# Kernel optimization log

Measured on AMD Instinct MI355X. Metric: run time of the kernel, lower is better.

## Reference

```python
import jax, jax.numpy as jnp
import numpy as np

L, D, H, FF = 4, 256, 8, 4 * 256  # num_layers, d_model, nhead, ffn hidden
DK = D // H
EPS = 1e-5


def _ln(x, g, b):
    mu = jnp.mean(x, axis=-1, keepdims=True)
    var = jnp.mean(jnp.square(x - mu), axis=-1, keepdims=True)
    return (x - mu) * jax.lax.rsqrt(var + EPS) * g + b


def setup_inputs() -> dict:
    key = jax.random.key(0)
    ks = jax.random.split(key, 16)
    B, N = 8, 1024
    s = 0.02
    return {
        "x": jax.random.normal(ks[0], (B, N, D), jnp.float32),
        "coords": jax.random.normal(ks[1], (B, N, 3), jnp.float32),
        "Wq": jax.random.normal(ks[2], (L, D, D), jnp.float32) * s,
        "bq": jnp.zeros((L, D), jnp.float32),
        "Wk": jax.random.normal(ks[3], (L, D, D), jnp.float32) * s,
        "bk": jnp.zeros((L, D), jnp.float32),
        "Wv": jax.random.normal(ks[4], (L, D, D), jnp.float32) * s,
        "bv": jnp.zeros((L, D), jnp.float32),
        "alpha": jnp.full((L,), 0.1, jnp.float32),
        "W1": jax.random.normal(ks[5], (L, D, FF), jnp.float32) * s,
        "b1": jnp.zeros((L, FF), jnp.float32),
        "W2": jax.random.normal(ks[6], (L, FF, D), jnp.float32) * s,
        "b2": jnp.zeros((L, D), jnp.float32),
        "g1": jnp.ones((L, D), jnp.float32),
        "be1": jnp.zeros((L, D), jnp.float32),
        "g2": jnp.ones((L, D), jnp.float32),
        "be2": jnp.zeros((L, D), jnp.float32),
    }


def reference(x, coords, Wq, bq, Wk, bk, Wv, bv, alpha, W1, b1, W2, b2, g1, be1, g2, be2):
    B, N, _ = x.shape
    # Per-batch pairwise coord dot products (same math as the BN x BN matmul
    # sliced per batch in the original, computed without the cross-batch waste).
    G0 = jnp.einsum("bnc,bmc->bnm", coords, coords)  # [B,N,N]
    scale = 1.0 / jnp.sqrt(jnp.float32(DK))
    for i in range(L):
        q = (x @ Wq[i] + bq[i]).reshape(B, N, H, DK)
        k = (x @ Wk[i] + bk[i]).reshape(B, N, H, DK)
        v = (x @ Wv[i] + bv[i]).reshape(B, N, H, DK)
        scores = jnp.einsum("bnhd,bmhd->bhnm", q, k) * scale + (alpha[i] * G0)[:, None]
        attn = jax.nn.softmax(scores, axis=-1)
        out = jnp.einsum("bhnm,bmhd->bnhd", attn, v).reshape(B, N, D)
        x = _ln(x + out, g1[i], be1[i])
        ff = jnp.maximum(x @ W1[i] + b1[i], 0.0) @ W2[i] + b2[i]
        x = _ln(x + ff, g2[i], be2[i])
    return x
```

## Files before the change

kernel.cpp:

```cpp
#include <hip/hip_runtime.h>
#include <hip/hip_bf16.h>

#define BB 8
#define NN 1024
#define DD 256
#define HH 8
#define DK 32
#define FFN 1024
#define NLAYERS 4
#define MM (BB * NN)
#define ROW_ELEMS (MM * DD)

#define QSCALE 0.2550655192922103f
#define LOG2E  1.4426950408889634f

typedef unsigned short ushort_t;
typedef __attribute__((ext_vector_type(8))) short bf16x8;
typedef __attribute__((ext_vector_type(4))) short bf16x4;
typedef __attribute__((ext_vector_type(4))) float f32x4;

__device__ __forceinline__ f32x4 mfma16(bf16x4 a, bf16x4 b, f32x4 c) {
#if __has_builtin(__builtin_amdgcn_mfma_f32_16x16x16bf16_1k)
    return __builtin_amdgcn_mfma_f32_16x16x16bf16_1k(a, b, c, 0, 0, 0);
#elif defined(__AMDGCN__)
    f32x4 d;
    asm volatile("v_mfma_f32_16x16x16_bf16 %0, %1, %2, %3"
                 : "=v"(d)
                 : "v"(a), "v"(b), "v"(c));
    return d;
#else
    return c;
#endif
}

__device__ __forceinline__ ushort_t f2b(float f) {
    __hip_bfloat16 h = __float2bfloat16(f);
    return *reinterpret_cast<ushort_t*>(&h);
}

__device__ __forceinline__ float fast_exp2(float x) {
#if __has_builtin(__builtin_amdgcn_exp2f)
    return __builtin_amdgcn_exp2f(x);
#else
    return exp2f(x);
#endif
}

__device__ __forceinline__ void async_ld16(const void* g, void* l) {
    __builtin_amdgcn_global_load_lds((const __attribute__((address_space(1))) void*)g,
                                     (__attribute__((address_space(3))) void*)l, 16, 0, 0);
}

__global__ __launch_bounds__(256) void copy_in_kernel(const float4* __restrict__ in,
                                                      float4* __restrict__ xf,
                                                      ushort4* __restrict__ xb, int n4,
                                                      const float* __restrict__ coords,
                                                      ushort_t* __restrict__ Qa,
                                                      ushort_t* __restrict__ Ka) {
    int i = blockIdx.x * 256 + threadIdx.x;
    if (i < n4) {
        float4 v = in[i];
        xf[i] = v;
        ushort4 b = {f2b(v.x), f2b(v.y), f2b(v.z), f2b(v.w)};
        xb[i] = b;
    }
    if (blockIdx.x < 256) {
        const int id = blockIdx.x * 256 + threadIdx.x;
        const int bh = id >> 10, n = id & 1023;
        const int b = bh >> 3;
        ushort_t buf[32];
#pragma unroll
        for (int d = 0; d < 32; ++d) buf[d] = 0;
        buf[0] = f2b(coords[(size_t)(b * NN + n) * 3 + 0]);
        buf[1] = f2b(coords[(size_t)(b * NN + n) * 3 + 1]);
        buf[2] = f2b(coords[(size_t)(b * NN + n) * 3 + 2]);
        ushort_t* kp = Ka + ((size_t)bh * NN + n) * 64 + 32;
        ushort_t* qp = Qa + ((size_t)bh * NN + n) * 64 + 32;
        const uint4* b4 = (const uint4*)buf;
        uint4 z4 = {0u, 0u, 0u, 0u};
#pragma unroll
        for (int c = 0; c < 4; ++c) {
            *(uint4*)(kp + c * 8) = b4[c];
            *(uint4*)(qp + c * 8) = z4;
        }
    }
}

__global__ __launch_bounds__(256) void prep_kernel(const float* __restrict__ Wq,
                                                   const float* __restrict__ Wk,
                                                   const float* __restrict__ Wv,
                                                   const float* __restrict__ W1,
                                                   const float* __restrict__ W2,
                                                   const float* __restrict__ bq,
                                                   const float* __restrict__ bk,
                                                   const float* __restrict__ bv,
                                                   ushort_t* __restrict__ wqkvt,
                                                   ushort_t* __restrict__ w1t,
                                                   ushort_t* __restrict__ w2t,
                                                   float* __restrict__ bqkv) {
    const int id = blockIdx.x;
    const int layer = id / 707;
    const int r = id % 707;
    const int tid = threadIdx.x;

    if (r >= 704) {
        const int chunk = r - 704;
        const float* src = (chunk == 0) ? bq : (chunk == 1) ? bk : bv;
        bqkv[layer * 768 + chunk * 256 + tid] = src[layer * 256 + tid];
        return;
    }

    const float* src;
    ushort_t* dst;
    int R, C, x, y;
    if (r < 192) {
        const int w = r >> 6, rr = r & 63;
        src = ((w == 0) ? Wq : (w == 1) ? Wk : Wv) + (size_t)layer * 65536;
        dst = wqkvt + (size_t)layer * 196608 + w * 65536;
        R = 256; C = 256; x = rr & 7; y = rr >> 3;
    } else if (r < 448) {
        const int rr = r - 192;
        src = W1 + (size_t)layer * 262144;
        dst = w1t + (size_t)layer * 262144;
        R = 256; C = 1024; x = rr & 31; y = rr >> 5;
    } else {
        const int rr = r - 448;
        src = W2 + (size_t)layer * 262144;
        dst = w2t + (size_t)layer * 262144;
        R = 1024; C = 256; x = rr & 7; y = rr >> 3;
    }
    const int r0 = y * 32, c0 = x * 32;
    __shared__ float tile[32][33];
    const int tx = tid & 31, ty = tid >> 5;
#pragma unroll
    for (int i = 0; i < 4; ++i)
        tile[ty + 8 * i][tx] = src[(size_t)(r0 + ty + 8 * i) * C + (c0 + tx)];
    __syncthreads();
#pragma unroll
    for (int i = 0; i < 4; ++i)
        dst[(size_t)(c0 + ty + 8 * i) * R + (r0 + tx)] = f2b(tile[tx][ty + 8 * i]);
}

template <int MODE, int BM>
__global__ __launch_bounds__(256) void mfma_gemm_kernel(const ushort_t* __restrict__ A,
                                                        const ushort_t* __restrict__ Bt,
                                                        const float* __restrict__ bias,
                                                        void* __restrict__ C0,
                                                        void* __restrict__ C1,
                                                        void* __restrict__ C2,
                                                        const float* __restrict__ coords,
                                                        const float* __restrict__ alpha, int layer,
                                                        int K, int ldc) {
    constexpr int NI = BM / 32;
    __shared__ ushort_t As0[2][BM * 32];
    __shared__ ushort_t As1[2][BM * 32];
    __shared__ ushort_t Bs0[2][128 * 32];
    __shared__ ushort_t Bs1[2][128 * 32];

    const int t    = threadIdx.x;
    const int bm   = blockIdx.y * BM;
    const int bn   = blockIdx.x * 128;
    const int wave = t >> 6, lane = t & 63;
    const int wm   = (wave >> 1) * (BM / 2), wn = (wave & 1) * 64;
    const int quad = lane >> 4, l16 = lane & 15;

    const int srow = t >> 2;
    const int scol = (t & 3) * 8;

    f32x4 acc[NI][4];
#pragma unroll
    for (int i = 0; i < NI; ++i)
#pragma unroll
        for (int j = 0; j < 4; ++j) {
            f32x4 z = {0.f, 0.f, 0.f, 0.f};
            acc[i][j] = z;
        }

    auto stage = [&](int pb, int k0) {
        async_ld16(A + (size_t)(bm + srow) * K + k0 + scol, As0[pb] + wave * 512);
        if constexpr (BM == 128)
            async_ld16(A + (size_t)(bm + 64 + srow) * K + k0 + scol, As0[pb] + 2048 + wave * 512);
        async_ld16(Bt + (size_t)(bn + srow) * K + k0 + scol, Bs0[pb] + wave * 512);
        async_ld16(Bt + (size_t)(bn + 64 + srow) * K + k0 + scol, Bs0[pb] + 2048 + wave * 512);
        async_ld16(A + (size_t)(bm + srow) * K + k0 + 32 + scol, As1[pb] + wave * 512);
        if constexpr (BM == 128)
            async_ld16(A + (size_t)(bm + 64 + srow) * K + k0 + 32 + scol, As1[pb] + 2048 + wave * 512);
        async_ld16(Bt + (size_t)(bn + srow) * K + k0 + 32 + scol, Bs1[pb] + wave * 512);
        async_ld16(Bt + (size_t)(bn + 64 + srow) * K + k0 + 32 + scol, Bs1[pb] + 2048 + wave * 512);
    };

    stage(0, 0);
    int pb = 0;
    for (int k0 = 0; k0 < K; k0 += 64, pb ^= 1) {
        __syncthreads();

        if (k0 + 64 < K) stage(pb ^ 1, k0 + 64);

        bf16x8 af0[NI], af1[NI], bf0[4], bf1[4];
#pragma unroll
        for (int i = 0; i < NI; ++i) {
            af0[i] = *(const bf16x8*)(As0[pb] + (wm + i * 16 + l16) * 32 + quad * 8);
            af1[i] = *(const bf16x8*)(As1[pb] + (wm + i * 16 + l16) * 32 + quad * 8);
        }
#pragma unroll
        for (int j = 0; j < 4; ++j) {
            bf0[j] = *(const bf16x8*)(Bs0[pb] + (wn + j * 16 + l16) * 32 + quad * 8);
            bf1[j] = *(const bf16x8*)(Bs1[pb] + (wn + j * 16 + l16) * 32 + quad * 8);
        }
#pragma unroll
        for (int i = 0; i < NI; ++i)
#pragma unroll
            for (int j = 0; j < 4; ++j) {
                acc[i][j] = __builtin_amdgcn_mfma_f32_16x16x32_bf16(af0[i], bf0[j], acc[i][j], 0, 0, 0);
                acc[i][j] = __builtin_amdgcn_mfma_f32_16x16x32_bf16(af1[i], bf1[j], acc[i][j], 0, 0, 0);
            }
    }

    const float av = (MODE == 2) ? alpha[layer] : 0.f;

#pragma unroll
    for (int j = 0; j < 4; ++j) {
        const int col = bn + wn + j * 16 + l16;
        const float bsv = bias[col];
#pragma unroll
        for (int i = 0; i < NI; ++i) {
            const int row0 = bm + wm + i * 16 + quad * 4;
            if (MODE == 2) {
                const int bb2 = row0 >> 10, nn0 = row0 & 1023;
                const int which = col >> 8, rem = col & 255;
                const int h = rem >> 5, d = rem & 31;
                const size_t bh = (size_t)((bb2 << 3) + h);
                if (which == 2) {
                    ushort4 pk;
                    pk.x = f2b(acc[i][j][0] + bsv);
                    pk.y = f2b(acc[i][j][1] + bsv);
                    pk.z = f2b(acc[i][j][2] + bsv);
                    pk.w = f2b(acc[i][j][3] + bsv);
                    *(ushort4*)&((ushort_t*)C2)[(bh * DK + d) * NN + nn0] = pk;
                } else {
#pragma unroll
                    for (int r = 0; r < 4; ++r) {
                        const float v = acc[i][j][r] + bsv;
                        const int nn = nn0 + r;
                        if (which == 0) {
                            ((ushort_t*)C0)[(bh * NN + nn) * 64 + d] = f2b(v * QSCALE);
                            if (d < 3)
                                ((ushort_t*)C0)[(bh * NN + nn) * 64 + 32 + d] =
                                    f2b(av * LOG2E * coords[(size_t)(bb2 * NN + nn) * 3 + d]);
                        } else {
                            ((ushort_t*)C1)[(bh * NN + nn) * 64 + d] = f2b(v);
                        }
                    }
                }
            } else {
#pragma unroll
                for (int r = 0; r < 4; ++r) {
                    float v = acc[i][j][r] + bsv;
                    if (MODE == 0)
                        ((float*)C0)[(size_t)(row0 + r) * ldc + col] = v;
                    else
                        ((ushort_t*)C0)[(size_t)(row0 + r) * ldc + col] = f2b(fmaxf(v, 0.f));
                }
            }
        }
    }
}

template <int DO_QKV>
__global__ __launch_bounds__(512) void ffn_ln_kernel(const float* __restrict__ aout,
                                                     const float* __restrict__ xfin,
                                                     const ushort_t* __restrict__ W1t,
                                                     const ushort_t* __restrict__ W2t,
                                                     const float* __restrict__ g1,
                                                     const float* __restrict__ be1,
                                                     const float* __restrict__ b1,
                                                     const float* __restrict__ b2,
                                                     const float* __restrict__ g2,
                                                     const float* __restrict__ be2,
                                                     float* __restrict__ xout,
                                                     const ushort_t* __restrict__ Wqkvt,
                                                     const float* __restrict__ bqkv,
                                                     const float* __restrict__ coords,
                                                     const float* __restrict__ alpha, int qlayer,
                                                     ushort_t* __restrict__ Qa,
                                                     ushort_t* __restrict__ Ka,
                                                     ushort_t* __restrict__ Vt) {
    __shared__ ushort_t Ha[8][32][32];
    __shared__ ushort_t Asf[8][32][32];
    __shared__ ushort_t Bs0[2][256 * 32];
    __shared__ ushort_t Bs1[2][256 * 32];
    __shared__ float Ya[32][260];
    __shared__ float redS[8][32];
    __shared__ float redQ[8][32];

    const int t = threadIdx.x;
    const int bm = blockIdx.x * 32;
    const int wave = t >> 6, lane = t & 63;
    const int quad = lane >> 4, l16 = lane & 15;
    const int wn = wave * 32;
    const int scol = (t & 3) * 8;

    auto stageB1 = [&](int pb, int nc, int ks) {
        const int nbase = nc * 256;
        const int k0 = ks * 64;
#pragma unroll
        for (int c = 0; c < 2; ++c) {
            const int brow = nbase + c * 128 + (t >> 2);
            async_ld16(W1t + (size_t)brow * 256 + k0 + scol, Bs0[pb] + c * 4096 + wave * 512);
            async_ld16(W1t + (size_t)brow * 256 + k0 + 32 + scol, Bs1[pb] + c * 4096 + wave * 512);
        }
    };
    auto stageB2 = [&](int pb, int nc, int ks) {
        const int k0 = nc * 256 + ks * 64;
#pragma unroll
        for (int c = 0; c < 2; ++c) {
            const int brow = c * 128 + (t >> 2);
            async_ld16(W2t + (size_t)brow * 1024 + k0 + scol, Bs0[pb] + c * 4096 + wave * 512);
            async_ld16(W2t + (size_t)brow * 1024 + k0 + 32 + scol, Bs1[pb] + c * 4096 + wave * 512);
        }
    };
    auto stage = [&](int pb, int st) {
        const int group = st >> 2, ks = st & 3, nc = group >> 1;
        if (!(group & 1)) stageB1(pb, nc, ks);
        else stageB2(pb, nc, ks);
    };
    auto stageQKV = [&](int pb, int qst) {
        const int chunk = qst >> 2, ks = qst & 3;
#pragma unroll
        for (int c = 0; c < 2; ++c) {
            const int brow = chunk * 256 + c * 128 + (t >> 2);
            async_ld16(Wqkvt + (size_t)brow * 256 + ks * 64 + scol, Bs0[pb] + c * 4096 + wave * 512);
            async_ld16(Wqkvt + (size_t)brow * 256 + ks * 64 + 32 + scol, Bs1[pb] + c * 4096 + wave * 512);
        }
    };

    stage(0, 0);

#pragma unroll
    for (int rr = 0; rr < 4; ++rr) {
        const int row = wave * 4 + rr;
        const size_t base = (size_t)(bm + row) * DD + lane * 4;

        float4 xv = *(const float4*)(xfin + base);
        float4 dl = *(const float4*)(aout + base);
        float v0 = xv.x + dl.x, v1 = xv.y + dl.y, v2 = xv.z + dl.z, v3 = xv.w + dl.w;

        float s = v0 + v1 + v2 + v3;
#pragma unroll
        for (int off = 32; off; off >>= 1) s += __shfl_xor(s, off);
        const float mean = s * (1.0f / 256.0f);

        float d0 = v0 - mean, d1 = v1 - mean, d2 = v2 - mean, d3 = v3 - mean;
        float s2 = d0 * d0 + d1 * d1 + d2 * d2 + d3 * d3;
#pragma unroll
        for (int off = 32; off; off >>= 1) s2 += __shfl_xor(s2, off);
        const float rs = rsqrtf(s2 * (1.0f / 256.0f) + 1e-5f);

        float4 gv = *(const float4*)(g1 + lane * 4);
        float4 bv = *(const float4*)(be1 + lane * 4);
        float y0 = d0 * rs * gv.x + bv.x;
        float y1 = d1 * rs * gv.y + bv.y;
        float y2 = d2 * rs * gv.z + bv.z;
        float y3 = d3 * rs * gv.w + bv.w;

        float4 yv = {y0, y1, y2, y3};
        *(float4*)&Ya[row][lane * 4] = yv;
        const int col0 = lane * 4;
        ushort4 yb = {f2b(y0), f2b(y1), f2b(y2), f2b(y3)};
        *(ushort4*)&Asf[col0 >> 5][row][col0 & 31] = yb;
    }

    f32x4 acc1[2][2], acc2[2][2];
#pragma unroll
    for (int i = 0; i < 2; ++i)
#pragma unroll
        for (int j = 0; j < 2; ++j) {
            f32x4 z = {0.f, 0.f, 0.f, 0.f};
            acc1[i][j] = z;
            acc2[i][j] = z;
        }

    int pb = 0;
    for (int st = 0; st < 32; ++st, pb ^= 1) {
        __syncthreads();
        if (st < 31) stage(pb ^ 1, st + 1);
        else if (DO_QKV) stageQKV(pb ^ 1, 0);

        const int group = st >> 2, ks = st & 3;
        const bool ff1 = !(group & 1);

        bf16x8 af0[2], af1[2], bf0[2], bf1[2];
#pragma unroll
        for (int i = 0; i < 2; ++i) {
            if (ff1) {
                af0[i] = *(const bf16x8*)&Asf[2 * ks][i * 16 + l16][quad * 8];
                af1[i] = *(const bf16x8*)&Asf[2 * ks + 1][i * 16 + l16][quad * 8];
            } else {
                af0[i] = *(const bf16x8*)&Ha[2 * ks][i * 16 + l16][quad * 8];
                af1[i] = *(const bf16x8*)&Ha[2 * ks + 1][i * 16 + l16][quad * 8];
            }
        }
#pragma unroll
        for (int j = 0; j < 2; ++j) {
            bf0[j] = *(const bf16x8*)(Bs0[pb] + (wn + j * 16 + l16) * 32 + quad * 8);
            bf1[j] = *(const bf16x8*)(Bs1[pb] + (wn + j * 16 + l16) * 32 + quad * 8);
        }

        if (ff1) {
#pragma unroll
            for (int i = 0; i < 2; ++i)
#pragma unroll
                for (int j = 0; j < 2; ++j) {
                    acc1[i][j] = __builtin_amdgcn_mfma_f32_16x16x32_bf16(af0[i], bf0[j], acc1[i][j], 0, 0, 0);
                    acc1[i][j] = __builtin_amdgcn_mfma_f32_16x16x32_bf16(af1[i], bf1[j], acc1[i][j], 0, 0, 0);
                }
            if (ks == 3) {
                const int nc = group >> 1;
#pragma unroll
                for (int j = 0; j < 2; ++j) {
                    const int col = nc * 256 + wn + j * 16 + l16;
                    const float bj = b1[col];
#pragma unroll
                    for (int i = 0; i < 2; ++i)
#pragma unroll
                        for (int r = 0; r < 4; ++r) {
                            const int row = i * 16 + quad * 4 + r;
                            Ha[wave][row][j * 16 + l16] =
                                f2b(fmaxf(acc1[i][j][r] + bj, 0.f));
                        }
                }
#pragma unroll
                for (int i = 0; i < 2; ++i)
#pragma unroll
                    for (int j = 0; j < 2; ++j) {
                        f32x4 z = {0.f, 0.f, 0.f, 0.f};
                        acc1[i][j] = z;
                    }
            }
        } else {
#pragma unroll
            for (int i = 0; i < 2; ++i)
#pragma unroll
                for (int j = 0; j < 2; ++j) {
                    acc2[i][j] = __builtin_amdgcn_mfma_f32_16x16x32_bf16(af0[i], bf0[j], acc2[i][j], 0, 0, 0);
                    acc2[i][j] = __builtin_amdgcn_mfma_f32_16x16x32_bf16(af1[i], bf1[j], acc2[i][j], 0, 0, 0);
                }
        }
    }

    float mean[2][4], rstd[2][4];

    {
        float sum_[2][4];
#pragma unroll
        for (int i = 0; i < 2; ++i)
#pragma unroll
            for (int r = 0; r < 4; ++r) sum_[i][r] = 0.f;
#pragma unroll
        for (int j = 0; j < 2; ++j) {
            const int col = wn + j * 16 + l16;
            const float bj = b2[col];
#pragma unroll
            for (int i = 0; i < 2; ++i) {
#pragma unroll
                for (int r = 0; r < 4; ++r) {
                    const int row = i * 16 + quad * 4 + r;
                    const float v = acc2[i][j][r] + bj + Ya[row][col];
                    acc2[i][j][r] = v;
                    sum_[i][r] += v;
                }
            }
        }
#pragma unroll
        for (int i = 0; i < 2; ++i)
#pragma unroll
            for (int r = 0; r < 4; ++r) {
                float s = sum_[i][r];
                s += __shfl_xor(s, 1);
                s += __shfl_xor(s, 2);
                s += __shfl_xor(s, 4);
                s += __shfl_xor(s, 8);
                sum_[i][r] = s;
            }
        if (l16 == 0) {
#pragma unroll
            for (int i = 0; i < 2; ++i)
#pragma unroll
                for (int r = 0; r < 4; ++r) redS[wave][i * 16 + quad * 4 + r] = sum_[i][r];
        }
        __syncthreads();
#pragma unroll
        for (int i = 0; i < 2; ++i)
#pragma unroll
            for (int r = 0; r < 4; ++r) {
                const int rl = i * 16 + quad * 4 + r;
                float s = 0.f;
#pragma unroll
                for (int w = 0; w < 8; ++w) s += redS[w][rl];
                mean[i][r] = s * (1.0f / 256.0f);
            }
    }

    {
        float sq_[2][4];
#pragma unroll
        for (int i = 0; i < 2; ++i)
#pragma unroll
            for (int r = 0; r < 4; ++r) sq_[i][r] = 0.f;
#pragma unroll
        for (int j = 0; j < 2; ++j)
#pragma unroll
            for (int i = 0; i < 2; ++i)
#pragma unroll
                for (int r = 0; r < 4; ++r) {
                    const float d = acc2[i][j][r] - mean[i][r];
                    sq_[i][r] += d * d;
                }
#pragma unroll
        for (int i = 0; i < 2; ++i)
#pragma unroll
            for (int r = 0; r < 4; ++r) {
                float s = sq_[i][r];
                s += __shfl_xor(s, 1);
                s += __shfl_xor(s, 2);
                s += __shfl_xor(s, 4);
                s += __shfl_xor(s, 8);
                sq_[i][r] = s;
            }
        if (l16 == 0) {
#pragma unroll
            for (int i = 0; i < 2; ++i)
#pragma unroll
                for (int r = 0; r < 4; ++r) redQ[wave][i * 16 + quad * 4 + r] = sq_[i][r];
        }
        __syncthreads();
#pragma unroll
        for (int i = 0; i < 2; ++i)
#pragma unroll
            for (int r = 0; r < 4; ++r) {
                const int rl = i * 16 + quad * 4 + r;
                float s = 0.f;
#pragma unroll
                for (int w = 0; w < 8; ++w) s += redQ[w][rl];
                rstd[i][r] = rsqrtf(s * (1.0f / 256.0f) + 1e-5f);
            }
    }

#pragma unroll
    for (int j = 0; j < 2; ++j) {
        const int col = wn + j * 16 + l16;
        const float gv = g2[col];
        const float bev = be2[col];
#pragma unroll
        for (int i = 0; i < 2; ++i) {
            const int row = bm + i * 16 + quad * 4;
#pragma unroll
            for (int r = 0; r < 4; ++r) {
                const float y = (acc2[i][j][r] - mean[i][r]) * rstd[i][r] * gv + bev;
                xout[(size_t)(row + r) * DD + col] = y;
                if (DO_QKV)
                    Asf[wave][i * 16 + quad * 4 + r][j * 16 + l16] = f2b(y);
            }
        }
    }

    if constexpr (DO_QKV) {
        const float av = alpha[qlayer];
        f32x4 acc3[2][2];
#pragma unroll
        for (int i = 0; i < 2; ++i)
#pragma unroll
            for (int j = 0; j < 2; ++j) {
                f32x4 z = {0.f, 0.f, 0.f, 0.f};
                acc3[i][j] = z;
            }

        for (int qst = 0; qst < 12; ++qst, pb ^= 1) {
            __syncthreads();
            if (qst < 11) stageQKV(pb ^ 1, qst + 1);

            const int ks = qst & 3;
            bf16x8 af0[2], af1[2], bf0[2], bf1[2];
#pragma unroll
            for (int i = 0; i < 2; ++i) {
                af0[i] = *(const bf16x8*)&Asf[2 * ks][i * 16 + l16][quad * 8];
                af1[i] = *(const bf16x8*)&Asf[2 * ks + 1][i * 16 + l16][quad * 8];
            }
#pragma unroll
            for (int j = 0; j < 2; ++j) {
                bf0[j] = *(const bf16x8*)(Bs0[pb] + (wn + j * 16 + l16) * 32 + quad * 8);
                bf1[j] = *(const bf16x8*)(Bs1[pb] + (wn + j * 16 + l16) * 32 + quad * 8);
            }
#pragma unroll
            for (int i = 0; i < 2; ++i)
#pragma unroll
                for (int j = 0; j < 2; ++j) {
                    acc3[i][j] = __builtin_amdgcn_mfma_f32_16x16x32_bf16(af0[i], bf0[j], acc3[i][j], 0, 0, 0);
                    acc3[i][j] = __builtin_amdgcn_mfma_f32_16x16x32_bf16(af1[i], bf1[j], acc3[i][j], 0, 0, 0);
                }

            if (ks == 3) {
                const int which = qst >> 2;
#pragma unroll
                for (int j = 0; j < 2; ++j) {
                    const int rem = wn + j * 16 + l16;
                    const float bsv = bqkv[which * 256 + rem];
                    const int h = rem >> 5, d = rem & 31;
#pragma unroll
                    for (int i = 0; i < 2; ++i) {
                        const int row0 = bm + i * 16 + quad * 4;
                        const int bb2 = row0 >> 10, nn0 = row0 & 1023;
                        const size_t bh = (size_t)((bb2 << 3) + h);
                        if (which == 2) {
                            ushort4 pk;
                            pk.x = f2b(acc3[i][j][0] + bsv);
                            pk.y = f2b(acc3[i][j][1] + bsv);
                            pk.z = f2b(acc3[i][j][2] + bsv);
                            pk.w = f2b(acc3[i][j][3] + bsv);
                            *(ushort4*)&Vt[(bh * DK + d) * NN + nn0] = pk;
                        } else {
#pragma unroll
                            for (int r = 0; r < 4; ++r) {
                                const float v = acc3[i][j][r] + bsv;
                                const int nn = nn0 + r;
                                if (which == 0) {
                                    Qa[(bh * NN + nn) * 64 + d] = f2b(v * QSCALE);
                                    if (d < 3)
                                        Qa[(bh * NN + nn) * 64 + 32 + d] =
                                            f2b(av * LOG2E *
                                                coords[(size_t)(bb2 * NN + nn) * 3 + d]);
                                } else {
                                    Ka[(bh * NN + nn) * 64 + d] = f2b(v);
                                }
                            }
                        }
                    }
                }
#pragma unroll
                for (int i = 0; i < 2; ++i)
#pragma unroll
                    for (int j = 0; j < 2; ++j) {
                        f32x4 z = {0.f, 0.f, 0.f, 0.f};
                        acc3[i][j] = z;
                    }
            }
        }
    }
}

__global__ __launch_bounds__(256, 2) void attn8_kernel(const ushort_t* __restrict__ Qa,
                                                       const ushort_t* __restrict__ Ka,
                                                       const ushort_t* __restrict__ Vt,
                                                       float* __restrict__ aout) {
    const int b = blockIdx.x, h = blockIdx.y, n0 = blockIdx.z * 64;
    const int t = threadIdx.x, wave = t >> 6, lane = t & 63;
    const int quad = lane >> 4, l16 = lane & 15;
    const int bh = b * HH + h;

    __shared__ __align__(16) char smem[56320];
    ushort_t (*Ks)[64][72] = (ushort_t (*)[64][72])smem;
    ushort_t (*Vs)[32][72] = (ushort_t (*)[32][72])(smem + 36864);
    float    (*Om)[64][36] = (float (*)[64][36])smem;
    float    (*Lm)[64]     = (float (*)[64])(smem + 55296);

    bf16x8 aq[4][2];
#pragma unroll
    for (int s = 0; s < 4; ++s) {
        const ushort_t* qp = Qa + ((size_t)bh * NN + n0 + s * 16 + l16) * 64 + quad * 8;
        aq[s][0] = *(const bf16x8*)qp;
        aq[s][1] = *(const bf16x8*)(qp + 32);
    }

    const f32x4 z = {0.f, 0.f, 0.f, 0.f};
    f32x4 acc[4][2];
    float lsum[4];
#pragma unroll
    for (int s = 0; s < 4; ++s) { acc[s][0] = z; acc[s][1] = z; lsum[s] = 0.f; }

    const ushort_t* kg = Ka + ((size_t)bh * NN + wave * 256) * 64;
    const ushort_t* vg = Vt + (size_t)bh * DK * NN + wave * 256;

    const int srow = lane >> 3, sch = (lane & 7) * 8;

    uint4 kreg[8], vreg[4];
#pragma unroll
    for (int i = 0; i < 8; ++i) kreg[i] = *(const uint4*)(kg + (size_t)(i * 8 + srow) * 64 + sch);
#pragma unroll
    for (int i = 0; i < 4; ++i) vreg[i] = *(const uint4*)(vg + (size_t)(i * 8 + srow) * NN + sch);

    for (int kt = 0; kt < 4; ++kt) {
#pragma unroll
        for (int i = 0; i < 8; ++i) *(uint4*)&Ks[wave][i * 8 + srow][sch] = kreg[i];
#pragma unroll
        for (int i = 0; i < 4; ++i) *(uint4*)&Vs[wave][i * 8 + srow][sch] = vreg[i];

        bf16x8 bk0[4], bk1[4];
#pragma unroll
        for (int jt = 0; jt < 4; ++jt) {
            bk0[jt] = *(const bf16x8*)&Ks[wave][jt * 16 + l16][quad * 8];
            bk1[jt] = *(const bf16x8*)&Ks[wave][jt * 16 + l16][32 + quad * 8];
        }
        bf16x4 vfrag[2][4];
#pragma unroll
        for (int g = 0; g < 2; ++g)
#pragma unroll
            for (int jt = 0; jt < 4; ++jt)
                vfrag[g][jt] = *(const bf16x4*)&Vs[wave][g * 16 + l16][jt * 16 + quad * 4];

        if (kt < 3) {
            const ushort_t* kg2 = kg + (size_t)(kt + 1) * 64 * 64;
            const ushort_t* vg2 = vg + (kt + 1) * 64;
#pragma unroll
            for (int i = 0; i < 8; ++i)
                kreg[i] = *(const uint4*)(kg2 + (size_t)(i * 8 + srow) * 64 + sch);
#pragma unroll
            for (int i = 0; i < 4; ++i)
                vreg[i] = *(const uint4*)(vg2 + (size_t)(i * 8 + srow) * NN + sch);
        }

#pragma unroll
        for (int s = 0; s < 4; ++s) {
            f32x4 st[4];
            __builtin_amdgcn_s_setprio(1);
#pragma unroll
            for (int jt = 0; jt < 4; ++jt) {
                st[jt] = __builtin_amdgcn_mfma_f32_16x16x32_bf16(bk0[jt], aq[s][0], z, 0, 0, 0);
                st[jt] = __builtin_amdgcn_mfma_f32_16x16x32_bf16(bk1[jt], aq[s][1], st[jt], 0, 0, 0);
            }
            __builtin_amdgcn_s_setprio(0);
            bf16x4 pf[4];
            float ls = 0.f;
#pragma unroll
            for (int jt = 0; jt < 4; ++jt) {
                float e0 = fast_exp2(st[jt][0]);
                float e1 = fast_exp2(st[jt][1]);
                float e2 = fast_exp2(st[jt][2]);
                float e3 = fast_exp2(st[jt][3]);
                ls += (e0 + e1) + (e2 + e3);
                pf[jt][0] = (short)f2b(e0);
                pf[jt][1] = (short)f2b(e1);
                pf[jt][2] = (short)f2b(e2);
                pf[jt][3] = (short)f2b(e3);
            }
            lsum[s] += ls;
            __builtin_amdgcn_s_setprio(1);
#pragma unroll
            for (int jt = 0; jt < 4; ++jt) {
                acc[s][0] = mfma16(vfrag[0][jt], pf[jt], acc[s][0]);
                acc[s][1] = mfma16(vfrag[1][jt], pf[jt], acc[s][1]);
            }
            __builtin_amdgcn_s_setprio(0);
        }
    }

#pragma unroll
    for (int s = 0; s < 4; ++s) {
        lsum[s] += __shfl_xor(lsum[s], 16);
        lsum[s] += __shfl_xor(lsum[s], 32);
    }

    __syncthreads();
    if (quad == 0) {
#pragma unroll
        for (int s = 0; s < 4; ++s) Lm[wave][s * 16 + l16] = lsum[s];
    }

#pragma unroll
    for (int s = 0; s < 4; ++s) {
        const int q = s * 16 + l16;
#pragma unroll
        for (int g = 0; g < 2; ++g) {
            float4 v = {acc[s][g][0], acc[s][g][1], acc[s][g][2], acc[s][g][3]};
            *(float4*)&Om[wave][q][g * 16 + quad * 4] = v;
        }
    }
    __syncthreads();

    {
        const int q = t >> 2, dseg = (t & 3) * 8;
        const float inv = 1.0f / (Lm[0][q] + Lm[1][q] + Lm[2][q] + Lm[3][q]);
        float* op = aout + (size_t)(b * NN + n0 + q) * DD + h * DK + dseg;
        float4 s0 = {0.f, 0.f, 0.f, 0.f}, s1 = {0.f, 0.f, 0.f, 0.f};
#pragma unroll
        for (int w = 0; w < 4; ++w) {
            float4 a = *(const float4*)&Om[w][q][dseg];
            float4 c = *(const float4*)&Om[w][q][dseg + 4];
            s0.x += a.x; s0.y += a.y; s0.z += a.z; s0.w += a.w;
            s1.x += c.x; s1.y += c.y; s1.z += c.z; s1.w += c.w;
        }
        float4 o0 = {s0.x * inv, s0.y * inv, s0.z * inv, s0.w * inv};
        float4 o1 = {s1.x * inv, s1.y * inv, s1.z * inv, s1.w * inv};
        *(float4*)op = o0;
        *(float4*)(op + 4) = o1;
    }
}

extern "C" void kernel_launch(void* const* d_in, const int* in_sizes, int n_in,
                              void* d_out, int out_size, void* d_ws, size_t ws_size,
                              hipStream_t stream) {
    const float* x      = (const float*)d_in[0];
    const float* coords = (const float*)d_in[1];
    const float* Wq     = (const float*)d_in[2];
    const float* bq     = (const float*)d_in[3];
    const float* Wk     = (const float*)d_in[4];
    const float* bk     = (const float*)d_in[5];
    const float* Wv     = (const float*)d_in[6];
    const float* bv     = (const float*)d_in[7];
    const float* alpha  = (const float*)d_in[8];
    const float* W1     = (const float*)d_in[9];
    const float* b1     = (const float*)d_in[10];
    const float* W2     = (const float*)d_in[11];
    const float* b2     = (const float*)d_in[12];
    const float* g1     = (const float*)d_in[13];
    const float* be1    = (const float*)d_in[14];
    const float* g2     = (const float*)d_in[15];
    const float* be2    = (const float*)d_in[16];

    float* ws = (float*)d_ws;
    float*    xf    = ws;
    ushort_t* xb    = (ushort_t*)(ws + 2097152);
    ushort_t* Qa    = (ushort_t*)(ws + 3145728);
    ushort_t* Ka    = (ushort_t*)(ws + 5242880);
    ushort_t* Vt    = (ushort_t*)(ws + 7340032);
    float*    aout  = ws + 8388608;
    ushort_t* wqkvt = (ushort_t*)(ws + 10485760);
    ushort_t* w1t   = (ushort_t*)(ws + 10878976);
    ushort_t* w2t   = (ushort_t*)(ws + 11403264);
    float*    bqkv  = ws + 11927552;

    prep_kernel<<<NLAYERS * 707, 256, 0, stream>>>(Wq, Wk, Wv, W1, W2, bq, bk, bv,
                                                   wqkvt, w1t, w2t, bqkv);

    copy_in_kernel<<<ROW_ELEMS / 4 / 256, 256, 0, stream>>>(
        (const float4*)x, (float4*)xf, (ushort4*)xb, ROW_ELEMS / 4, coords, Qa, Ka);

    mfma_gemm_kernel<2, 64><<<dim3(6, 128), 256, 0, stream>>>(
        xb, wqkvt, bqkv, Qa, Ka, Vt, coords, alpha, 0, 256, 0);

    for (int i = 0; i < NLAYERS; ++i) {
        attn8_kernel<<<dim3(8, 8, 16), 256, 0, stream>>>(Qa, Ka, Vt, aout);

        if (i < NLAYERS - 1) {
            ffn_ln_kernel<1><<<MM / 32, 512, 0, stream>>>(
                aout, xf, w1t + (size_t)i * 262144, w2t + (size_t)i * 262144,
                g1 + i * 256, be1 + i * 256, b1 + i * 1024, b2 + i * 256,
                g2 + i * 256, be2 + i * 256, xf,
                wqkvt + (size_t)(i + 1) * 196608, bqkv + (i + 1) * 768,
                coords, alpha, i + 1, Qa, Ka, Vt);
        } else {
            ffn_ln_kernel<0><<<MM / 32, 512, 0, stream>>>(
                aout, xf, w1t + (size_t)i * 262144, w2t + (size_t)i * 262144,
                g1 + i * 256, be1 + i * 256, b1 + i * 1024, b2 + i * 256,
                g2 + i * 256, be2 + i * 256, (float*)d_out,
                nullptr, nullptr, nullptr, nullptr, 0, nullptr, nullptr, nullptr);
        }
    }
}
```

Before: 363.4 us.

## Triple-buffer weight staging in fused FFN/QKV kernel with partial vmcnt waits

Moves the FFN and QKV weight streaming from a double-buffered to a triple-buffered LDS pipeline, issuing loads two stages ahead. It replaces full __syncthreads with explicit s_waitcnt vmcnt(4) barriers, so the in-flight prefetch for the next stage is not drained each iteration. To fit the extra buffer in LDS, the reduction scratch is aliased onto the Ha array and the Ya padding is dropped. This risks LDS bank conflicts from the unpadded Ya rows and correctness problems if the vmcnt counting or the aliasing of Ha is wrong. The larger LDS footprint could also lower occupancy.

```diff
diff --git a/kernel.cpp b/kernel.cpp
--- a/kernel.cpp
+++ b/kernel.cpp
@@ -49,6 +49,21 @@
 __device__ __forceinline__ void async_ld16(const void* g, void* l) {
     __builtin_amdgcn_global_load_lds((const __attribute__((address_space(1))) void*)g,
                                      (__attribute__((address_space(3))) void*)l, 16, 0, 0);
+}
+
+__device__ __forceinline__ void pipe_barrier4() {
+#if defined(__AMDGCN__)
+    asm volatile("s_waitcnt vmcnt(4) lgkmcnt(0)" ::: "memory");
+#endif
+    __builtin_amdgcn_s_barrier();
+    __builtin_amdgcn_sched_barrier(0);
+}
+__device__ __forceinline__ void pipe_barrier0() {
+#if defined(__AMDGCN__)
+    asm volatile("s_waitcnt vmcnt(0) lgkmcnt(0)" ::: "memory");
+#endif
+    __builtin_amdgcn_s_barrier();
+    __builtin_amdgcn_sched_barrier(0);
 }
 
 __global__ __launch_bounds__(256) void copy_in_kernel(const float4* __restrict__ in,
@@ -287,11 +302,11 @@
                                                      ushort_t* __restrict__ Vt) {
     __shared__ ushort_t Ha[8][32][32];
     __shared__ ushort_t Asf[8][32][32];
-    __shared__ ushort_t Bs0[2][256 * 32];
-    __shared__ ushort_t Bs1[2][256 * 32];
-    __shared__ float Ya[32][260];
-    __shared__ float redS[8][32];
-    __shared__ float redQ[8][32];
+    __shared__ ushort_t Bs0[3][8192];
+    __shared__ ushort_t Bs1[3][8192];
+    __shared__ float Ya[32][256];
+    float* redS = (float*)&Ha[0][0][0];
+    float* redQ = redS + 256;
 
     const int t = threadIdx.x;
     const int bm = blockIdx.x * 32;
@@ -300,41 +315,42 @@
     const int wn = wave * 32;
     const int scol = (t & 3) * 8;
 
-    auto stageB1 = [&](int pb, int nc, int ks) {
+    auto stageB1 = [&](int buf, int nc, int ks) {
         const int nbase = nc * 256;
         const int k0 = ks * 64;
 #pragma unroll
         for (int c = 0; c < 2; ++c) {
             const int brow = nbase + c * 128 + (t >> 2);
-            async_ld16(W1t + (size_t)brow * 256 + k0 + scol, Bs0[pb] + c * 4096 + wave * 512);
-            async_ld16(W1t + (size_t)brow * 256 + k0 + 32 + scol, Bs1[pb] + c * 4096 + wave * 512);
+            async_ld16(W1t + (size_t)brow * 256 + k0 + scol, Bs0[buf] + c * 4096 + wave * 512);
+            async_ld16(W1t + (size_t)brow * 256 + k0 + 32 + scol, Bs1[buf] + c * 4096 + wave * 512);
         }
     };
-    auto stageB2 = [&](int pb, int nc, int ks) {
+    auto stageB2 = [&](int buf, int nc, int ks) {
         const int k0 = nc * 256 + ks * 64;
 #pragma unroll
         for (int c = 0; c < 2; ++c) {
             const int brow = c * 128 + (t >> 2);
-            async_ld16(W2t + (size_t)brow * 1024 + k0 + scol, Bs0[pb] + c * 4096 + wave * 512);
-            async_ld16(W2t + (size_t)brow * 1024 + k0 + 32 + scol, Bs1[pb] + c * 4096 + wave * 512);
+            async_ld16(W2t + (size_t)brow * 1024 + k0 + scol, Bs0[buf] + c * 4096 + wave * 512);
+            async_ld16(W2t + (size_t)brow * 1024 + k0 + 32 + scol, Bs1[buf] + c * 4096 + wave * 512);
         }
     };
-    auto stage = [&](int pb, int st) {
+    auto stageFFN = [&](int buf, int st) {
         const int group = st >> 2, ks = st & 3, nc = group >> 1;
-        if (!(group & 1)) stageB1(pb, nc, ks);
-        else stageB2(pb, nc, ks);
+        if (!(group & 1)) stageB1(buf, nc, ks);
+        else stageB2(buf, nc, ks);
     };
-    auto stageQKV = [&](int pb, int qst) {
+    auto stageQKV = [&](int buf, int qst) {
         const int chunk = qst >> 2, ks = qst & 3;
 #pragma unroll
         for (int c = 0; c < 2; ++c) {
             const int brow = chunk * 256 + c * 128 + (t >> 2);
-            async_ld16(Wqkvt + (size_t)brow * 256 + ks * 64 + scol, Bs0[pb] + c * 4096 + wave * 512);
-            async_ld16(Wqkvt + (size_t)brow * 256 + ks * 64 + 32 + scol, Bs1[pb] + c * 4096 + wave * 512);
+            async_ld16(Wqkvt + (size_t)brow * 256 + ks * 64 + scol, Bs0[buf] + c * 4096 + wave * 512);
+            async_ld16(Wqkvt + (size_t)brow * 256 + ks * 64 + 32 + scol, Bs1[buf] + c * 4096 + wave * 512);
         }
     };
 
-    stage(0, 0);
+    stageFFN(0, 0);
+    stageFFN(1, 1);
 
 #pragma unroll
     for (int rr = 0; rr < 4; ++rr) {
@@ -380,12 +396,15 @@
             acc2[i][j] = z;
         }
 
-    int pb = 0;
-    for (int st = 0; st < 32; ++st, pb ^= 1) {
-        __syncthreads();
-        if (st < 31) stage(pb ^ 1, st + 1);
-        else if (DO_QKV) stageQKV(pb ^ 1, 0);
-
+    for (int st = 0; st < 32; ++st) {
+        if (!DO_QKV && st == 31) pipe_barrier0();
+        else pipe_barrier4();
+
+        const int nxt = st + 2;
+        if (nxt < 32) stageFFN(nxt % 3, nxt);
+        else if (DO_QKV && nxt < 34) stageQKV(nxt % 3, nxt - 32);
+
+        const int buf = st % 3;
         const int group = st >> 2, ks = st & 3;
         const bool ff1 = !(group & 1);
 
@@ -402,8 +421,8 @@
         }
 #pragma unroll
         for (int j = 0; j < 2; ++j) {
-            bf0[j] = *(const bf16x8*)(Bs0[pb] + (wn + j * 16 + l16) * 32 + quad * 8);
-            bf1[j] = *(const bf16x8*)(Bs1[pb] + (wn + j * 16 + l16) * 32 + quad * 8);
+            bf0[j] = *(const bf16x8*)(Bs0[buf] + (wn + j * 16 + l16) * 32 + quad * 8);
+            bf1[j] = *(const bf16x8*)(Bs1[buf] + (wn + j * 16 + l16) * 32 + quad * 8);
         }
 
         if (ff1) {
@@ -449,6 +468,8 @@
     }
 
     float mean[2][4], rstd[2][4];
+
+    __syncthreads();
 
     {
         float sum_[2][4];
@@ -486,7 +507,7 @@
 #pragma unroll
             for (int i = 0; i < 2; ++i)
 #pragma unroll
-                for (int r = 0; r < 4; ++r) redS[wave][i * 16 + quad * 4 + r] = sum_[i][r];
+                for (int r = 0; r < 4; ++r) redS[wave * 32 + i * 16 + quad * 4 + r] = sum_[i][r];
         }
         __syncthreads();
 #pragma unroll
@@ -496,7 +517,7 @@
                 const int rl = i * 16 + quad * 4 + r;
                 float s = 0.f;
 #pragma unroll
-                for (int w = 0; w < 8; ++w) s += redS[w][rl];
+                for (int w = 0; w < 8; ++w) s += redS[w * 32 + rl];
                 mean[i][r] = s * (1.0f / 256.0f);
             }
     }
@@ -531,7 +552,7 @@
 #pragma unroll
             for (int i = 0; i < 2; ++i)
 #pragma unroll
-                for (int r = 0; r < 4; ++r) redQ[wave][i * 16 + quad * 4 + r] = sq_[i][r];
+                for (int r = 0; r < 4; ++r) redQ[wave * 32 + i * 16 + quad * 4 + r] = sq_[i][r];
         }
         __syncthreads();
 #pragma unroll
@@ -541,7 +562,7 @@
                 const int rl = i * 16 + quad * 4 + r;
                 float s = 0.f;
 #pragma unroll
-                for (int w = 0; w < 8; ++w) s += redQ[w][rl];
+                for (int w = 0; w < 8; ++w) s += redQ[w * 32 + rl];
                 rstd[i][r] = rsqrtf(s * (1.0f / 256.0f) + 1e-5f);
             }
     }
@@ -575,10 +596,14 @@
                 acc3[i][j] = z;
             }
 
-        for (int qst = 0; qst < 12; ++qst, pb ^= 1) {
-            __syncthreads();
-            if (qst < 11) stageQKV(pb ^ 1, qst + 1);
-
+        for (int qst = 0; qst < 12; ++qst) {
+            if (qst == 11) pipe_barrier0();
+            else pipe_barrier4();
+
+            const int gq = qst + 2;
+            if (gq < 12) stageQKV((32 + gq) % 3, gq);
+
+            const int buf = (32 + qst) % 3;
             const int ks = qst & 3;
             bf16x8 af0[2], af1[2], bf0[2], bf1[2];
 #pragma unroll
@@ -588,8 +613,8 @@
             }
 #pragma unroll
             for (int j = 0; j < 2; ++j) {
-                bf0[j] = *(const bf16x8*)(Bs0[pb] + (wn + j * 16 + l16) * 32 + quad * 8);
-                bf1[j] = *(const bf16x8*)(Bs1[pb] + (wn + j * 16 + l16) * 32 + quad * 8);
+                bf0[j] = *(const bf16x8*)(Bs0[buf] + (wn + j * 16 + l16) * 32 + quad * 8);
+                bf1[j] = *(const bf16x8*)(Bs1[buf] + (wn + j * 16 + l16) * 32 + quad * 8);
             }
 #pragma unroll
             for (int i = 0; i < 2; ++i)
```

Result: slower. 399.2 us (+9.9%).

## Double ffn_ln block to 1024 threads, one 16-column tile per wave

Applied to the files above, without the earlier changes.

The fused FFN+LayerNorm(+next-layer QKV) kernel now launches 16 waves per block instead of 8. Each wave owns a 16-wide column slice instead of 32, so per-wave accumulators and B-fragment loads are halved, and the LayerNorm reductions sum over 16 wave partials. The goal is more waves in flight to hide LDS and MFMA latency and to ease register pressure. In exchange, each wave reloads the A fragments for half as much MFMA work, block-wide barriers span twice as many waves, and the launch bound of 1024 threads with a minimum of 4 blocks may limit registers per thread.

```diff
diff --git a/kernel.cpp b/kernel.cpp
--- a/kernel.cpp
+++ b/kernel.cpp
@@ -267,78 +267,68 @@
 }
 
 template <int DO_QKV>
-__global__ __launch_bounds__(512) void ffn_ln_kernel(const float* __restrict__ aout,
-                                                     const float* __restrict__ xfin,
-                                                     const ushort_t* __restrict__ W1t,
-                                                     const ushort_t* __restrict__ W2t,
-                                                     const float* __restrict__ g1,
-                                                     const float* __restrict__ be1,
-                                                     const float* __restrict__ b1,
-                                                     const float* __restrict__ b2,
-                                                     const float* __restrict__ g2,
-                                                     const float* __restrict__ be2,
-                                                     float* __restrict__ xout,
-                                                     const ushort_t* __restrict__ Wqkvt,
-                                                     const float* __restrict__ bqkv,
-                                                     const float* __restrict__ coords,
-                                                     const float* __restrict__ alpha, int qlayer,
-                                                     ushort_t* __restrict__ Qa,
-                                                     ushort_t* __restrict__ Ka,
-                                                     ushort_t* __restrict__ Vt) {
+__global__ __launch_bounds__(1024, 4) void ffn_ln_kernel(const float* __restrict__ aout,
+                                                         const float* __restrict__ xfin,
+                                                         const ushort_t* __restrict__ W1t,
+                                                         const ushort_t* __restrict__ W2t,
+                                                         const float* __restrict__ g1,
+                                                         const float* __restrict__ be1,
+                                                         const float* __restrict__ b1,
+                                                         const float* __restrict__ b2,
+                                                         const float* __restrict__ g2,
+                                                         const float* __restrict__ be2,
+                                                         float* __restrict__ xout,
+                                                         const ushort_t* __restrict__ Wqkvt,
+                                                         const float* __restrict__ bqkv,
+                                                         const float* __restrict__ coords,
+                                                         const float* __restrict__ alpha, int qlayer,
+                                                         ushort_t* __restrict__ Qa,
+                                                         ushort_t* __restrict__ Ka,
+                                                         ushort_t* __restrict__ Vt) {
     __shared__ ushort_t Ha[8][32][32];
     __shared__ ushort_t Asf[8][32][32];
     __shared__ ushort_t Bs0[2][256 * 32];
     __shared__ ushort_t Bs1[2][256 * 32];
     __shared__ float Ya[32][260];
-    __shared__ float redS[8][32];
-    __shared__ float redQ[8][32];
+    __shared__ float redS[16][32];
+    __shared__ float redQ[16][32];
 
     const int t = threadIdx.x;
     const int bm = blockIdx.x * 32;
     const int wave = t >> 6, lane = t & 63;
     const int quad = lane >> 4, l16 = lane & 15;
-    const int wn = wave * 32;
+    const int wn = wave * 16;
     const int scol = (t & 3) * 8;
 
     auto stageB1 = [&](int pb, int nc, int ks) {
-        const int nbase = nc * 256;
+        const int brow = nc * 256 + (t >> 2);
         const int k0 = ks * 64;
-#pragma unroll
-        for (int c = 0; c < 2; ++c) {
-            const int brow = nbase + c * 128 + (t >> 2);
-            async_ld16(W1t + (size_t)brow * 256 + k0 + scol, Bs0[pb] + c * 4096 + wave * 512);
-            async_ld16(W1t + (size_t)brow * 256 + k0 + 32 + scol, Bs1[pb] + c * 4096 + wave * 512);
-        }
+        async_ld16(W1t + (size_t)brow * 256 + k0 + scol, Bs0[pb] + wave * 512);
+        async_ld16(W1t + (size_t)brow * 256 + k0 + 32 + scol, Bs1[pb] + wave * 512);
     };
     auto stageB2 = [&](int pb, int nc, int ks) {
+        const int brow = t >> 2;
         const int k0 = nc * 256 + ks * 64;
-#pragma unroll
-        for (int c = 0; c < 2; ++c) {
-            const int brow = c * 128 + (t >> 2);
-            async_ld16(W2t + (size_t)brow * 1024 + k0 + scol, Bs0[pb] + c * 4096 + wave * 512);
-            async_ld16(W2t + (size_t)brow * 1024 + k0 + 32 + scol, Bs1[pb] + c * 4096 + wave * 512);
-        }
+        async_ld16(W2t + (size_t)brow * 1024 + k0 + scol, Bs0[pb] + wave * 512);
+        async_ld16(W2t + (size_t)brow * 1024 + k0 + 32 + scol, Bs1[pb] + wave * 512);
     };
-    auto stage = [&](int pb, int st) {
+    auto stageFFN = [&](int pb, int st) {
         const int group = st >> 2, ks = st & 3, nc = group >> 1;
         if (!(group & 1)) stageB1(pb, nc, ks);
         else stageB2(pb, nc, ks);
     };
     auto stageQKV = [&](int pb, int qst) {
         const int chunk = qst >> 2, ks = qst & 3;
-#pragma unroll
-        for (int c = 0; c < 2; ++c) {
-            const int brow = chunk * 256 + c * 128 + (t >> 2);
-            async_ld16(Wqkvt + (size_t)brow * 256 + ks * 64 + scol, Bs0[pb] + c * 4096 + wave * 512);
-            async_ld16(Wqkvt + (size_t)brow * 256 + ks * 64 + 32 + scol, Bs1[pb] + c * 4096 + wave * 512);
-        }
+        const int brow = chunk * 256 + (t >> 2);
+        async_ld16(Wqkvt + (size_t)brow * 256 + ks * 64 + scol, Bs0[pb] + wave * 512);
+        async_ld16(Wqkvt + (size_t)brow * 256 + ks * 64 + 32 + scol, Bs1[pb] + wave * 512);
     };
 
-    stage(0, 0);
-
-#pragma unroll
-    for (int rr = 0; rr < 4; ++rr) {
-        const int row = wave * 4 + rr;
+    stageFFN(0, 0);
+
+#pragma unroll
+    for (int rr = 0; rr < 2; ++rr) {
+        const int row = wave * 2 + rr;
         const size_t base = (size_t)(bm + row) * DD + lane * 4;
 
         float4 xv = *(const float4*)(xfin + base);
@@ -370,26 +360,24 @@
         *(ushort4*)&Asf[col0 >> 5][row][col0 & 31] = yb;
     }
 
-    f32x4 acc1[2][2], acc2[2][2];
-#pragma unroll
-    for (int i = 0; i < 2; ++i)
-#pragma unroll
-        for (int j = 0; j < 2; ++j) {
-            f32x4 z = {0.f, 0.f, 0.f, 0.f};
-            acc1[i][j] = z;
-            acc2[i][j] = z;
-        }
+    f32x4 acc1[2], acc2[2];
+#pragma unroll
+    for (int i = 0; i < 2; ++i) {
+        f32x4 z = {0.f, 0.f, 0.f, 0.f};
+        acc1[i] = z;
+        acc2[i] = z;
+    }
 
     int pb = 0;
     for (int st = 0; st < 32; ++st, pb ^= 1) {
         __syncthreads();
-        if (st < 31) stage(pb ^ 1, st + 1);
+        if (st < 31) stageFFN(pb ^ 1, st + 1);
         else if (DO_QKV) stageQKV(pb ^ 1, 0);
 
         const int group = st >> 2, ks = st & 3;
         const bool ff1 = !(group & 1);
 
-        bf16x8 af0[2], af1[2], bf0[2], bf1[2];
+        bf16x8 af0[2], af1[2], bf0, bf1;
 #pragma unroll
         for (int i = 0; i < 2; ++i) {
             if (ff1) {
@@ -400,51 +388,39 @@
                 af1[i] = *(const bf16x8*)&Ha[2 * ks + 1][i * 16 + l16][quad * 8];
             }
         }
-#pragma unroll
-        for (int j = 0; j < 2; ++j) {
-            bf0[j] = *(const bf16x8*)(Bs0[pb] + (wn + j * 16 + l16) * 32 + quad * 8);
-            bf1[j] = *(const bf16x8*)(Bs1[pb] + (wn + j * 16 + l16) * 32 + quad * 8);
-        }
+        bf0 = *(const bf16x8*)(Bs0[pb] + (wn + l16) * 32 + quad * 8);
+        bf1 = *(const bf16x8*)(Bs1[pb] + (wn + l16) * 32 + quad * 8);
 
         if (ff1) {
 #pragma unroll
-            for (int i = 0; i < 2; ++i)
-#pragma unroll
-                for (int j = 0; j < 2; ++j) {
-                    acc1[i][j] = __builtin_amdgcn_mfma_f32_16x16x32_bf16(af0[i], bf0[j], acc1[i][j], 0, 0, 0);
-                    acc1[i][j] = __builtin_amdgcn_mfma_f32_16x16x32_bf16(af1[i], bf1[j], acc1[i][j], 0, 0, 0);
-                }
+            for (int i = 0; i < 2; ++i) {
+                acc1[i] = __builtin_amdgcn_mfma_f32_16x16x32_bf16(af0[i], bf0, acc1[i], 0, 0, 0);
+                acc1[i] = __builtin_amdgcn_mfma_f32_16x16x32_bf16(af1[i], bf1, acc1[i], 0, 0, 0);
+            }
             if (ks == 3) {
                 const int nc = group >> 1;
-#pragma unroll
-                for (int j = 0; j < 2; ++j) {
-                    const int col = nc * 256 + wn + j * 16 + l16;
-                    const float bj = b1[col];
-#pragma unroll
-                    for (int i = 0; i < 2; ++i)
-#pragma unroll
-                        for (int r = 0; r < 4; ++r) {
-                            const int row = i * 16 + quad * 4 + r;
-                            Ha[wave][row][j * 16 + l16] =
-                                f2b(fmaxf(acc1[i][j][r] + bj, 0.f));
-                        }
+                const int col = nc * 256 + wn + l16;
+                const float bj = b1[col];
+#pragma unroll
+                for (int i = 0; i < 2; ++i)
+#pragma unroll
+                    for (int r = 0; r < 4; ++r) {
+                        const int row = i * 16 + quad * 4 + r;
+                        Ha[wave >> 1][row][(wave & 1) * 16 + l16] =
+                            f2b(fmaxf(acc1[i][r] + bj, 0.f));
+                    }
+#pragma unroll
+                for (int i = 0; i < 2; ++i) {
+                    f32x4 z = {0.f, 0.f, 0.f, 0.f};
+                    acc1[i] = z;
                 }
-#pragma unroll
-                for (int i = 0; i < 2; ++i)
-#pragma unroll
-                    for (int j = 0; j < 2; ++j) {
-                        f32x4 z = {0.f, 0.f, 0.f, 0.f};
-                        acc1[i][j] = z;
-                    }
             }
         } else {
 #pragma unroll
-            for (int i = 0; i < 2; ++i)
-#pragma unroll
-                for (int j = 0; j < 2; ++j) {
-                    acc2[i][j] = __builtin_amdgcn_mfma_f32_16x16x32_bf16(af0[i], bf0[j], acc2[i][j], 0, 0, 0);
-                    acc2[i][j] = __builtin_amdgcn_mfma_f32_16x16x32_bf16(af1[i], bf1[j], acc2[i][j], 0, 0, 0);
-                }
+            for (int i = 0; i < 2; ++i) {
+                acc2[i] = __builtin_amdgcn_mfma_f32_16x16x32_bf16(af0[i], bf0, acc2[i], 0, 0, 0);
+                acc2[i] = __builtin_amdgcn_mfma_f32_16x16x32_bf16(af1[i], bf1, acc2[i], 0, 0, 0);
+            }
         }
     }
 
@@ -456,19 +432,16 @@
         for (int i = 0; i < 2; ++i)
 #pragma unroll
             for (int r = 0; r < 4; ++r) sum_[i][r] = 0.f;
-#pragma unroll
-        for (int j = 0; j < 2; ++j) {
-            const int col = wn + j * 16 + l16;
-            const float bj = b2[col];
-#pragma unroll
-            for (int i = 0; i < 2; ++i) {
-#pragma unroll
-                for (int r = 0; r < 4; ++r) {
-                    const int row = i * 16 + quad * 4 + r;
-                    const float v = acc2[i][j][r] + bj + Ya[row][col];
-                    acc2[i][j][r] = v;
-                    sum_[i][r] += v;
-                }
+        const int col = wn + l16;
+        const float bj = b2[col];
+#pragma unroll
+        for (int i = 0; i < 2; ++i) {
+#pragma unroll
+            for (int r = 0; r < 4; ++r) {
+                const int row = i * 16 + quad * 4 + r;
+                const float v = acc2[i][r] + bj + Ya[row][col];
+                acc2[i][r] = v;
+                sum_[i][r] += v;
             }
         }
 #pragma unroll
@@ -496,7 +469,7 @@
                 const int rl = i * 16 + quad * 4 + r;
                 float s = 0.f;
 #pragma unroll
-                for (int w = 0; w < 8; ++w) s += redS[w][rl];
+                for (int w = 0; w < 16; ++w) s += redS[w][rl];
                 mean[i][r] = s * (1.0f / 256.0f);
             }
     }
@@ -506,16 +479,10 @@
 #pragma unroll
         for (int i = 0; i < 2; ++i)
 #pragma unroll
-            for (int r = 0; r < 4; ++r) sq_[i][r] = 0.f;
-#pragma unroll
-        for (int j = 0; j < 2; ++j)
-#pragma unroll
-            for (int i = 0; i < 2; ++i)
-#pragma unroll
-                for (int r = 0; r < 4; ++r) {
-                    const float d = acc2[i][j][r] - mean[i][r];
-                    sq_[i][r] += d * d;
-                }
+            for (int r = 0; r < 4; ++r) {
+                const float d = acc2[i][r] - mean[i][r];
+                sq_[i][r] = d * d;
+            }
 #pragma unroll
         for (int i = 0; i < 2; ++i)
 #pragma unroll
@@ -541,14 +508,13 @@
                 const int rl = i * 16 + quad * 4 + r;
                 float s = 0.f;
 #pragma unroll
-                for (int w = 0; w < 8; ++w) s += redQ[w][rl];
+                for (int w = 0; w < 16; ++w) s += redQ[w][rl];
                 rstd[i][r] = rsqrtf(s * (1.0f / 256.0f) + 1e-5f);
             }
     }
 
-#pragma unroll
-    for (int j = 0; j < 2; ++j) {
-        const int col = wn + j * 16 + l16;
+    {
+        const int col = wn + l16;
         const float gv = g2[col];
         const float bev = be2[col];
 #pragma unroll
@@ -556,93 +522,81 @@
             const int row = bm + i * 16 + quad * 4;
 #pragma unroll
             for (int r = 0; r < 4; ++r) {
-                const float y = (acc2[i][j][r] - mean[i][r]) * rstd[i][r] * gv + bev;
+                const float y = (acc2[i][r] - mean[i][r]) * rstd[i][r] * gv + bev;
                 xout[(size_t)(row + r) * DD + col] = y;
                 if (DO_QKV)
-                    Asf[wave][i * 16 + quad * 4 + r][j * 16 + l16] = f2b(y);
+                    Asf[wave >> 1][i * 16 + quad * 4 + r][(wave & 1) * 16 + l16] = f2b(y);
             }
         }
     }
 
     if constexpr (DO_QKV) {
         const float av = alpha[qlayer];
-        f32x4 acc3[2][2];
-#pragma unroll
-        for (int i = 0; i < 2; ++i)
-#pragma unroll
-            for (int j = 0; j < 2; ++j) {
-                f32x4 z = {0.f, 0.f, 0.f, 0.f};
-                acc3[i][j] = z;
-            }
+        f32x4 acc3[2];
+#pragma unroll
+        for (int i = 0; i < 2; ++i) {
+            f32x4 z = {0.f, 0.f, 0.f, 0.f};
+            acc3[i] = z;
+        }
 
         for (int qst = 0; qst < 12; ++qst, pb ^= 1) {
             __syncthreads();
             if (qst < 11) stageQKV(pb ^ 1, qst + 1);
 
             const int ks = qst & 3;
-            bf16x8 af0[2], af1[2], bf0[2], bf1[2];
+            bf16x8 af0[2], af1[2], bf0, bf1;
 #pragma unroll
             for (int i = 0; i < 2; ++i) {
                 af0[i] = *(const bf16x8*)&Asf[2 * ks][i * 16 + l16][quad * 8];
                 af1[i] = *(const bf16x8*)&Asf[2 * ks + 1][i * 16 + l16][quad * 8];
             }
-#pragma unroll
-            for (int j = 0; j < 2; ++j) {
-                bf0[j] = *(const bf16x8*)(Bs0[pb] + (wn + j * 16 + l16) * 32 + quad * 8);
-                bf1[j] = *(const bf16x8*)(Bs1[pb] + (wn + j * 16 + l16) * 32 + quad * 8);
-            }
-#pragma unroll
-            for (int i = 0; i < 2; ++i)
-#pragma unroll
-                for (int j = 0; j < 2; ++j) {
-                    acc3[i][j] = __builtin_amdgcn_mfma_f32_16x16x32_bf16(af0[i], bf0[j], acc3[i][j], 0, 0, 0);
-                    acc3[i][j] = __builtin_amdgcn_mfma_f32_16x16x32_bf16(af1[i], bf1[j], acc3[i][j], 0, 0, 0);
-                }
+            bf0 = *(const bf16x8*)(Bs0[pb] + (wn + l16) * 32 + quad * 8);
+            bf1 = *(const bf16x8*)(Bs1[pb] + (wn + l16) * 32 + quad * 8);
+#pragma unroll
+            for (int i = 0; i < 2; ++i) {
+                acc3[i] = __builtin_amdgcn_mfma_f32_16x16x32_bf16(af0[i], bf0, acc3[i], 0, 0, 0);
+                acc3[i] = __builtin_amdgcn_mfma_f32_16x16x32_bf16(af1[i], bf1, acc3[i], 0, 0, 0);
+            }
 
             if (ks == 3) {
                 const int which = qst >> 2;
-#pragma unroll
-                for (int j = 0; j < 2; ++j) {
-                    const int rem = wn + j * 16 + l16;
-                    const float bsv = bqkv[which * 256 + rem];
-                    const int h = rem >> 5, d = rem & 31;
-#pragma unroll
-                    for (int i = 0; i < 2; ++i) {
-                        const int row0 = bm + i * 16 + quad * 4;
-                        const int bb2 = row0 >> 10, nn0 = row0 & 1023;
-                        const size_t bh = (size_t)((bb2 << 3) + h);
-                        if (which == 2) {
-                            ushort4 pk;
-                            pk.x = f2b(acc3[i][j][0] + bsv);
-                            pk.y = f2b(acc3[i][j][1] + bsv);
-                            pk.z = f2b(acc3[i][j][2] + bsv);
-                            pk.w = f2b(acc3[i][j][3] + bsv);
-                            *(ushort4*)&Vt[(bh * DK + d) * NN + nn0] = pk;
-                        } else {
-#pragma unroll
-                            for (int r = 0; r < 4; ++r) {
-                                const float v = acc3[i][j][r] + bsv;
-                                const int nn = nn0 + r;
-                                if (which == 0) {
-                                    Qa[(bh * NN + nn) * 64 + d] = f2b(v * QSCALE);
-                                    if (d < 3)
-                                        Qa[(bh * NN + nn) * 64 + 32 + d] =
-                                            f2b(av * LOG2E *
-                                                coords[(size_t)(bb2 * NN + nn) * 3 + d]);
-                                } else {
-                                    Ka[(bh * NN + nn) * 64 + d] = f2b(v);
-                                }
+                const int rem = wn + l16;
+                const float bsv = bqkv[which * 256 + rem];
+                const int h = rem >> 5, d = rem & 31;
+#pragma unroll
+                for (int i = 0; i < 2; ++i) {
+                    const int row0 = bm + i * 16 + quad * 4;
+                    const int bb2 = row0 >> 10, nn0 = row0 & 1023;
+                    const size_t bh = (size_t)((bb2 << 3) + h);
+                    if (which == 2) {
+                        ushort4 pk;
+                        pk.x = f2b(acc3[i][0] + bsv);
+                        pk.y = f2b(acc3[i][1] + bsv);
+                        pk.z = f2b(acc3[i][2] + bsv);
+                        pk.w = f2b(acc3[i][3] + bsv);
+                        *(ushort4*)&Vt[(bh * DK + d) * NN + nn0] = pk;
+                    } else {
+#pragma unroll
+                        for (int r = 0; r < 4; ++r) {
+                            const float v = acc3[i][r] + bsv;
+                            const int nn = nn0 + r;
+                            if (which == 0) {
+                                Qa[(bh * NN + nn) * 64 + d] = f2b(v * QSCALE);
+                                if (d < 3)
+                                    Qa[(bh * NN + nn) * 64 + 32 + d] =
+                                        f2b(av * LOG2E *
+                                            coords[(size_t)(bb2 * NN + nn) * 3 + d]);
+                            } else {
+                                Ka[(bh * NN + nn) * 64 + d] = f2b(v);
                             }
                         }
                     }
                 }
 #pragma unroll
-                for (int i = 0; i < 2; ++i)
-#pragma unroll
-                    for (int j = 0; j < 2; ++j) {
-                        f32x4 z = {0.f, 0.f, 0.f, 0.f};
-                        acc3[i][j] = z;
-                    }
+                for (int i = 0; i < 2; ++i) {
+                    f32x4 z = {0.f, 0.f, 0.f, 0.f};
+                    acc3[i] = z;
+                }
             }
         }
     }
@@ -841,14 +795,14 @@
         attn8_kernel<<<dim3(8, 8, 16), 256, 0, stream>>>(Qa, Ka, Vt, aout);
 
         if (i < NLAYERS - 1) {
-            ffn_ln_kernel<1><<<MM / 32, 512, 0, stream>>>(
+            ffn_ln_kernel<1><<<MM / 32, 1024, 0, stream>>>(
                 aout, xf, w1t + (size_t)i * 262144, w2t + (size_t)i * 262144,
                 g1 + i * 256, be1 + i * 256, b1 + i * 1024, b2 + i * 256,
                 g2 + i * 256, be2 + i * 256, xf,
                 wqkvt + (size_t)(i + 1) * 196608, bqkv + (i + 1) * 768,
                 coords, alpha, i + 1, Qa, Ka, Vt);
         } else {
-            ffn_ln_kernel<0><<<MM / 32, 512, 0, stream>>>(
+            ffn_ln_kernel<0><<<MM / 32, 1024, 0, stream>>>(
                 aout, xf, w1t + (size_t)i * 262144, w2t + (size_t)i * 262144,
                 g1 + i * 256, be1 + i * 256, b1 + i * 1024, b2 + i * 256,
                 g2 + i * 256, be2 + i * 256, (float*)d_out,
```

Result: no change. 370.5 us (+1.9%).
